# Optimization experiments

Measured on AMD Instinct MI355X. Metric: run time of the kernel, lower is better.

The kernel has to match this reference:

```python
import jax, jax.numpy as jnp
import numpy as np

BN_EPS = 1e-5
BIND_CHAN = 4  # hparams.MODEL.LEARNABLE_OFFSET.BIND_CHAN


def conv1x1(x, w, b):
    # x: [B,C,H,W], w: [O,C], b: [O]
    return jnp.einsum('bchw,oc->bohw', x, w) + b[None, :, None, None]


def bn_train(x, gamma, beta):
    # training-mode batch norm over (B,H,W) per channel
    mean = jnp.mean(x, axis=(0, 2, 3), keepdims=True)
    var = jnp.var(x, axis=(0, 2, 3), keepdims=True)
    xn = (x - mean) * jax.lax.rsqrt(var + BN_EPS)
    return xn * gamma[None, :, None, None] + beta[None, :, None, None]


def displace_channel(x, offsets):
    # x: [B,C,H,W]; offsets: [C,2] (dy,dx) per channel, continuous.
    # out[b,c,y,x] = bilinear sample of x[b,c] at (y+dy_c, x+dx_c), zeros outside.
    B, C, H, W = x.shape
    dy, dx = offsets[:, 0], offsets[:, 1]
    fy, fx = jnp.floor(dy), jnp.floor(dx)
    wy, wx = dy - fy, dx - fx          # fractional weights, [C]
    iy, ix = fy.astype(jnp.int32), fx.astype(jnp.int32)
    chan = jnp.arange(C)[:, None, None]

    def shifted(oy, ox):
        ys = jnp.arange(H)[None, :] + oy[:, None]   # [C,H]
        xs = jnp.arange(W)[None, :] + ox[:, None]   # [C,W]
        valid = ((ys >= 0) & (ys < H))[:, :, None] & ((xs >= 0) & (xs < W))[:, None, :]
        ysc = jnp.clip(ys, 0, H - 1)
        xsc = jnp.clip(xs, 0, W - 1)
        g = x[:, chan, ysc[:, :, None], xsc[:, None, :]]   # [B,C,H,W]
        return g * valid.astype(x.dtype)[None]

    w00 = ((1 - wy) * (1 - wx))[None, :, None, None]
    w01 = ((1 - wy) * wx)[None, :, None, None]
    w10 = (wy * (1 - wx))[None, :, None, None]
    w11 = (wy * wx)[None, :, None, None]
    return (w00 * shifted(iy, ix) + w01 * shifted(iy, ix + 1)
            + w10 * shifted(iy + 1, ix) + w11 * shifted(iy + 1, ix + 1))


def setup_inputs() -> dict:
    key = jax.random.key(0)
    ks = jax.random.split(key, 12)
    B, Cin, H, W = 16, 64, 128, 128
    Cd, Cout = 128, 64
    n_off = Cd // BIND_CHAN  # 32
    s_in = 1.0 / np.sqrt(Cin)
    s_d = 1.0 / np.sqrt(Cd)
    return {
        'x': jax.random.normal(ks[0], (B, Cin, H, W), jnp.float32),
        'pre_w': jax.random.uniform(ks[1], (Cd, Cin), jnp.float32, -s_in, s_in),
        'pre_b': jax.random.uniform(ks[2], (Cd,), jnp.float32, -s_in, s_in),
        'post_w': jax.random.uniform(ks[3], (Cout, Cd), jnp.float32, -s_d, s_d),
        'post_b': jax.random.uniform(ks[4], (Cout,), jnp.float32, -s_d, s_d),
        'atten_w': jax.random.uniform(ks[5], (Cd, Cin), jnp.float32, -s_in, s_in),
        'atten_b': jax.random.uniform(ks[6], (Cd,), jnp.float32, -s_in, s_in),
        'atten_bn_g': jnp.ones((Cd,), jnp.float32),
        'atten_bn_b': jnp.zeros((Cd,), jnp.float32),
        'offsets': jax.random.normal(ks[7], (n_off, 2), jnp.float32) * 3.0,
        'bn_g': jnp.ones((Cout,), jnp.float32),
        'bn_b': jnp.zeros((Cout,), jnp.float32),
    }


def reference(x, pre_w, pre_b, post_w, post_b, atten_w, atten_b,
              atten_bn_g, atten_bn_b, offsets, bn_g, bn_b):
    # pre_offset conv1x1
    out_pre = conv1x1(x, pre_w, pre_b)                        # [B,Cd,H,W]
    # DisplaceChannel: each offset shared by BIND_CHAN consecutive channels
    off_per_chan = jnp.repeat(offsets, BIND_CHAN, axis=0)     # [Cd,2]
    out_dis = displace_channel(out_pre, off_per_chan)
    # Attention branch: conv1x1 -> BN -> Softplus -> SpaceNormalization
    a = conv1x1(x, atten_w, atten_b)
    a = bn_train(a, atten_bn_g, atten_bn_b)
    a = jax.nn.softplus(a)
    out_atten = a / jnp.sum(a, axis=(2, 3), keepdims=True)    # spatial normalization
    # post_offset conv1x1 on gated displaced features
    out_post = conv1x1(out_atten * out_dis, post_w, post_b)
    # residual (inplanes == outplanes, stride 1 -> no downsample) + BN + ReLU
    out_skip = x + out_post
    return jax.nn.relu(bn_train(out_skip, bn_g, bn_b))
```

## Files before the change

kernel.cpp:

```cpp
#include <hip/hip_runtime.h>

#define HWSZ   16384
#define CIN    64
#define CD     128
#define COUT   64
#define BN_EPS 1e-5f

typedef __attribute__((ext_vector_type(8))) short short8x;
typedef __attribute__((ext_vector_type(4))) float floatx4;

#define WS_ASTAT 25344
#define WS_OSTAT 27392
#define WS_BIG   32768
#define WS_TOTAL_BYTES ((size_t)(32768 + 16777216) * 4)

__device__ __forceinline__ unsigned short f2bf(float f) {
    unsigned int u = __float_as_uint(f);
    u += 0x7fff + ((u >> 16) & 1);
    return (unsigned short)(u >> 16);
}
__device__ __forceinline__ float bf2f(unsigned short s) {
    return __uint_as_float(((unsigned int)s) << 16);
}
__device__ __forceinline__ float softplus_fast(float x) {
    return fmaxf(x, 0.f) + __logf(1.f + __expf(-fabsf(x)));
}
__device__ __forceinline__ float block_reduce(float v, float* sc) {
    #pragma unroll
    for (int off = 32; off >= 1; off >>= 1) v += __shfl_xor(v, off, 64);
    int wv = threadIdx.x >> 6, ln = threadIdx.x & 63;
    int nw = blockDim.x >> 6;
    if (ln == 0) sc[wv] = v;
    __syncthreads();
    float r = ((int)threadIdx.x < nw) ? sc[threadIdx.x] : 0.f;
    r += __shfl_xor(r, 1, 64);
    r += __shfl_xor(r, 2, 64);
    r += __shfl_xor(r, 4, 64);
    return r;
}

__device__ __forceinline__ short8x cvt_w8(const float* src) {
    float4 f0 = *(const float4*)(src);
    float4 f1 = *(const float4*)(src + 4);
    short8x w;
    w[0] = (short)f2bf(f0.x); w[1] = (short)f2bf(f0.y);
    w[2] = (short)f2bf(f0.z); w[3] = (short)f2bf(f0.w);
    w[4] = (short)f2bf(f1.x); w[5] = (short)f2bf(f1.y);
    w[6] = (short)f2bf(f1.z); w[7] = (short)f2bf(f1.w);
    return w;
}

#define OBPAD 68

__device__ __forceinline__ void pre_write_lds(unsigned short* wbuf, int c, int wv,
                                              const float4 ld[4]) {
    #pragma unroll
    for (int k = 0; k < 4; ++k) {
        int px = wv * 16 + k * 4;
        wbuf[(px + 0) * 72 + c] = f2bf(ld[k].x);
        wbuf[(px + 1) * 72 + c] = f2bf(ld[k].y);
        wbuf[(px + 2) * 72 + c] = f2bf(ld[k].z);
        wbuf[(px + 3) * 72 + c] = f2bf(ld[k].w);
    }
}

__device__ __forceinline__ void pre_compute_tile(
        const unsigned short* buf, unsigned short* ob, int ln, int wv,
        const short8x wfrag[4][2], const float bv[4]) {
    floatx4 acc[4][4];
    #pragma unroll
    for (int oi = 0; oi < 4; ++oi)
        #pragma unroll
        for (int pi = 0; pi < 4; ++pi)
            acc[oi][pi] = floatx4{bv[oi], bv[oi], bv[oi], bv[oi]};
    #pragma unroll
    for (int kk = 0; kk < 2; ++kk)
        #pragma unroll
        for (int pi = 0; pi < 4; ++pi) {
            short8x xfrag = *(const short8x*)((const char*)buf +
                    (pi * 16 + (ln & 15)) * 144 + (kk * 32 + (ln >> 4) * 8) * 2);
            #pragma unroll
            for (int oi = 0; oi < 4; ++oi)
                acc[oi][pi] = __builtin_amdgcn_mfma_f32_16x16x32_bf16(
                        xfrag, wfrag[oi][kk], acc[oi][pi], 0, 0, 0);
        }
    #pragma unroll
    for (int oi = 0; oi < 4; ++oi) {
        int row = wv * 64 + oi * 16 + (ln & 15);
        #pragma unroll
        for (int pi = 0; pi < 4; ++pi) {
            int px = pi * 16 + (ln >> 4) * 4;
            ushort4 v;
            v.x = f2bf(acc[oi][pi][0]); v.y = f2bf(acc[oi][pi][1]);
            v.z = f2bf(acc[oi][pi][2]); v.w = f2bf(acc[oi][pi][3]);
            *(ushort4*)&ob[row * OBPAD + px] = v;
        }
    }
}

__global__ __launch_bounds__(256) void conv_pre_mfma(
        const float* __restrict__ x, const float* __restrict__ pre_w,
        const float* __restrict__ atten_w,
        const float* __restrict__ pre_b, const float* __restrict__ atten_b,
        unsigned short* __restrict__ out_pre, unsigned short* __restrict__ a_out,
        float* __restrict__ a_stats8) {
    __shared__ unsigned short xT[2][64 * 72];
    __shared__ unsigned short ob[256 * OBPAD];
    int t = threadIdx.x;
    int wv = t >> 6, ln = t & 63;
    int b = blockIdx.x >> 6;
    int poff = (blockIdx.x & 63) << 8;
    const float* xg = x + (size_t)b * CIN * HWSZ + poff;
    int c = ln;

    int o0 = wv * 64;
    short8x wfrag[4][2];
    #pragma unroll
    for (int oi = 0; oi < 4; ++oi)
        #pragma unroll
        for (int kk = 0; kk < 2; ++kk) {
            int row = o0 + oi * 16 + (ln & 15);
            int kcol = kk * 32 + (ln >> 4) * 8;
            const float* wsrc = (row < 128) ? (pre_w + row * 64)
                                            : (atten_w + (row - 128) * 64);
            wfrag[oi][kk] = cvt_w8(wsrc + kcol);
        }
    float bv[4];
    #pragma unroll
    for (int oi = 0; oi < 4; ++oi) {
        int og = o0 + oi * 16;
        bv[oi] = (og < 128) ? pre_b[og + (ln & 15)] : atten_b[og - 128 + (ln & 15)];
    }

    float asum[4] = {0.f, 0.f, 0.f, 0.f};
    float asq[4]  = {0.f, 0.f, 0.f, 0.f};

    float4 lda[4], ldb[4];
    #pragma unroll
    for (int k = 0; k < 4; ++k)
        lda[k] = *(const float4*)(xg + (size_t)c * HWSZ + 0 * 64 + wv * 16 + k * 4);
    pre_write_lds(xT[0], c, wv, lda);
    #pragma unroll
    for (int k = 0; k < 4; ++k)
        lda[k] = *(const float4*)(xg + (size_t)c * HWSZ + 1 * 64 + wv * 16 + k * 4);
    __syncthreads();

    #pragma unroll
    for (int tt = 0; tt < 4; ++tt) {
        if (tt == 0) {
            #pragma unroll
            for (int k = 0; k < 4; ++k)
                ldb[k] = *(const float4*)(xg + (size_t)c * HWSZ + 2 * 64 + wv * 16 + k * 4);
        } else if (tt == 1) {
            #pragma unroll
            for (int k = 0; k < 4; ++k)
                lda[k] = *(const float4*)(xg + (size_t)c * HWSZ + 3 * 64 + wv * 16 + k * 4);
        }
        pre_compute_tile(xT[tt & 1], ob, ln, wv, wfrag, bv);
        if (tt == 0)      pre_write_lds(xT[1], c, wv, lda);
        else if (tt == 1) pre_write_lds(xT[0], c, wv, ldb);
        else if (tt == 2) pre_write_lds(xT[1], c, wv, lda);
        __syncthreads();
        int ptile = poff + tt * 64;
        #pragma unroll
        for (int j = 0; j < 8; ++j) {
            int row = j * 32 + (t >> 3);
            int px  = (t & 7) * 8;
            uint4 v = *(const uint4*)&ob[row * OBPAD + px];
            unsigned short* dst = (row < 128) ? out_pre : a_out;
            int o = row & 127;
            *(uint4*)(dst + ((size_t)b * CD + o) * HWSZ + ptile + px) = v;
            if (j >= 4) {
                unsigned int u[4] = {v.x, v.y, v.z, v.w};
                float s = 0.f, q = 0.f;
                #pragma unroll
                for (int k = 0; k < 4; ++k) {
                    float lo = bf2f((unsigned short)(u[k] & 0xffff));
                    float hi = bf2f((unsigned short)(u[k] >> 16));
                    s += lo + hi;
                    q += lo * lo + hi * hi;
                }
                asum[j - 4] += s;
                asq[j - 4]  += q;
            }
        }
        __syncthreads();
    }
    float* slot = a_stats8 + (blockIdx.x & 7) * 256;
    #pragma unroll
    for (int jj = 0; jj < 4; ++jj) {
        float s = asum[jj], q = asq[jj];
        s += __shfl_xor(s, 1, 64); q += __shfl_xor(q, 1, 64);
        s += __shfl_xor(s, 2, 64); q += __shfl_xor(q, 2, 64);
        s += __shfl_xor(s, 4, 64); q += __shfl_xor(q, 4, 64);
        if ((t & 7) == 0) {
            int o = (jj + 4) * 32 + (t >> 3) - 128;
            atomicAdd(&slot[2 * o],     s);
            atomicAdd(&slot[2 * o + 1], q);
        }
    }
}

__global__ __launch_bounds__(256) void chan_stats_bf16(
        const unsigned short* __restrict__ src, float* __restrict__ stats) {
    __shared__ float sc1[8], sc2[8];
    int c = blockIdx.x, b = blockIdx.y;
    const unsigned short* base = src + ((size_t)b * CD + c) * HWSZ;
    int t = threadIdx.x;
    float sum = 0.f, sq = 0.f;
    #pragma unroll
    for (int i = 0; i < 8; ++i) {
        uint4 v = *(const uint4*)(base + i * 2048 + t * 8);
        unsigned int u[4] = {v.x, v.y, v.z, v.w};
        #pragma unroll
        for (int k = 0; k < 4; ++k) {
            float lo = bf2f((unsigned short)(u[k] & 0xffff));
            float hi = bf2f((unsigned short)(u[k] >> 16));
            sum += lo + hi;
            sq  += lo * lo + hi * hi;
        }
    }
    sum = block_reduce(sum, sc1);
    __syncthreads();
    sq = block_reduce(sq, sc2);
    if (t == 0) {
        atomicAdd(&stats[c * 2 + 0], sum);
        atomicAdd(&stats[c * 2 + 1], sq);
    }
}

struct Win9 { float v0,v1,v2,v3,v4,v5,v6,v7,v8; };
__device__ __forceinline__ Win9 extract9(uint4 qa, uint4 qb, bool s4, int sh) {
    unsigned long long A0 = ((unsigned long long)qa.y << 32) | qa.x;
    unsigned long long A1 = ((unsigned long long)qa.w << 32) | qa.z;
    unsigned long long A2 = ((unsigned long long)qb.y << 32) | qb.x;
    unsigned long long A3 = ((unsigned long long)qb.w << 32) | qb.z;
    unsigned long long B0 = s4 ? A1 : A0;
    unsigned long long B1 = s4 ? A2 : A1;
    unsigned long long B2 = s4 ? A3 : A2;
    unsigned long long r0 = sh ? ((B0 >> sh) | (B1 << (64 - sh))) : B0;
    unsigned long long r1 = sh ? ((B1 >> sh) | (B2 << (64 - sh))) : B1;
    unsigned int v8w = (unsigned int)(sh ? (B2 >> sh) : B2);
    Win9 w;
    w.v0 = bf2f((unsigned short)(r0 >>  0)); w.v1 = bf2f((unsigned short)(r0 >> 16));
    w.v2 = bf2f((unsigned short)(r0 >> 32)); w.v3 = bf2f((unsigned short)(r0 >> 48));
    w.v4 = bf2f((unsigned short)(r1 >>  0)); w.v5 = bf2f((unsigned short)(r1 >> 16));
    w.v6 = bf2f((unsigned short)(r1 >> 32)); w.v7 = bf2f((unsigned short)(r1 >> 48));
    w.v8 = bf2f((unsigned short)(v8w & 0xffff));
    return w;
}

__global__ __launch_bounds__(512) void displace_bnsp_mul(
        unsigned short* __restrict__ pre, const unsigned short* __restrict__ a_raw,
        const float* __restrict__ stats8, const float* __restrict__ g,
        const float* __restrict__ bb, const float* __restrict__ offsets) {
    __shared__ unsigned short img[128 * 136];
    __shared__ float sc[8];
    __shared__ float s_inv;
    int bc = blockIdx.x;
    int cc = bc & 127;
    float dy = offsets[(cc >> 2) * 2 + 0];
    float dx = offsets[(cc >> 2) * 2 + 1];
    float fy = floorf(dy), fx = floorf(dx);
    float wy = dy - fy, wx = dx - fx;
    int iy = (int)fy, ix = (int)fx;
    float w00 = (1.f - wy) * (1.f - wx);
    float w01 = (1.f - wy) * wx;
    float w10 = wy * (1.f - wx);
    float w11 = wy * wx;
    float sum = 0.f, sq = 0.f;
    #pragma unroll
    for (int k = 0; k < 8; ++k) {
        sum += stats8[k * 256 + 2 * cc];
        sq  += stats8[k * 256 + 2 * cc + 1];
    }
    const float N = 262144.f;
    float mean = sum / N;
    float var  = sq / N - mean * mean;
    float rstd = rsqrtf(var + BN_EPS);
    float scl = rstd * g[cc];
    float shf = bb[cc] - mean * scl;
    unsigned short* pb = pre + (size_t)bc * HWSZ;
    const unsigned short* ab = a_raw + (size_t)bc * HWSZ;
    int t = threadIdx.x;
    float aspf[4][8];
    float lsum = 0.f;
    #pragma unroll
    for (int i = 0; i < 4; ++i) {
        int px = i * 4096 + t * 8;
        uint4 v = *(const uint4*)(pb + px);
        int y = px >> 7, xx = px & 127;
        *(uint4*)&img[y * 136 + xx] = v;
        uint4 av = *(const uint4*)(ab + px);
        unsigned int au[4] = {av.x, av.y, av.z, av.w};
        #pragma unroll
        for (int k = 0; k < 4; ++k) {
            float lo = softplus_fast(bf2f((unsigned short)(au[k] & 0xffff)) * scl + shf);
            float hi = softplus_fast(bf2f((unsigned short)(au[k] >> 16))    * scl + shf);
            lsum += lo + hi;
            aspf[i][2 * k]     = lo;
            aspf[i][2 * k + 1] = hi;
        }
    }
    lsum = block_reduce(lsum, sc);
    if (t == 0) s_inv = 1.f / lsum;
    __syncthreads();
    float inv = s_inv;
    w00 *= inv; w01 *= inv; w10 *= inv; w11 *= inv;
    int s = ix & 7;
    int ix8 = ix - s;
    int sh = (s & 3) * 16;
    bool s4 = s >= 4;
    #pragma unroll
    for (int i = 0; i < 4; ++i) {
        int px = i * 4096 + t * 8;
        int y = px >> 7, x0 = px & 127;
        int yy0 = y + iy, yy1 = yy0 + 1;
        float wA0 = (yy0 >= 0 && yy0 < 128) ? w00 : 0.f;
        float wA1 = (yy0 >= 0 && yy0 < 128) ? w01 : 0.f;
        float wB0 = (yy1 >= 0 && yy1 < 128) ? w10 : 0.f;
        float wB1 = (yy1 >= 0 && yy1 < 128) ? w11 : 0.f;
        int yc0 = min(max(yy0, 0), 127), yc1 = min(max(yy1, 0), 127);
        int w0 = x0 + ix8;
        uint4 z = {0u, 0u, 0u, 0u};
        uint4 qa0 = (w0 >= 0 && w0 <= 120)         ? *(const uint4*)&img[yc0 * 136 + w0]     : z;
        uint4 qa1 = (w0 + 8 >= 0 && w0 + 8 <= 120) ? *(const uint4*)&img[yc0 * 136 + w0 + 8] : z;
        uint4 qb0 = (w0 >= 0 && w0 <= 120)         ? *(const uint4*)&img[yc1 * 136 + w0]     : z;
        uint4 qb1 = (w0 + 8 >= 0 && w0 + 8 <= 120) ? *(const uint4*)&img[yc1 * 136 + w0 + 8] : z;
        Win9 va = extract9(qa0, qa1, s4, sh);
        Win9 vb = extract9(qb0, qb1, s4, sh);
        float m0 = (wA0*va.v0 + wA1*va.v1 + wB0*vb.v0 + wB1*vb.v1) * aspf[i][0];
        float m1 = (wA0*va.v1 + wA1*va.v2 + wB0*vb.v1 + wB1*vb.v2) * aspf[i][1];
        float m2 = (wA0*va.v2 + wA1*va.v3 + wB0*vb.v2 + wB1*vb.v3) * aspf[i][2];
        float m3 = (wA0*va.v3 + wA1*va.v4 + wB0*vb.v3 + wB1*vb.v4) * aspf[i][3];
        float m4 = (wA0*va.v4 + wA1*va.v5 + wB0*vb.v4 + wB1*vb.v5) * aspf[i][4];
        float m5 = (wA0*va.v5 + wA1*va.v6 + wB0*vb.v5 + wB1*vb.v6) * aspf[i][5];
        float m6 = (wA0*va.v6 + wA1*va.v7 + wB0*vb.v6 + wB1*vb.v7) * aspf[i][6];
        float m7 = (wA0*va.v7 + wA1*va.v8 + wB0*vb.v7 + wB1*vb.v8) * aspf[i][7];
        uint4 o;
        o.x = (unsigned int)f2bf(m0) | ((unsigned int)f2bf(m1) << 16);
        o.y = (unsigned int)f2bf(m2) | ((unsigned int)f2bf(m3) << 16);
        o.z = (unsigned int)f2bf(m4) | ((unsigned int)f2bf(m5) << 16);
        o.w = (unsigned int)f2bf(m6) | ((unsigned int)f2bf(m7) << 16);
        *(uint4*)(pb + px) = o;
    }
}

__global__ __launch_bounds__(256) void conv_post_mfma(
        const unsigned short* __restrict__ m, const float* __restrict__ post_w,
        const float* __restrict__ post_b, const float* __restrict__ x,
        unsigned short* __restrict__ skipS) {
    __shared__ unsigned short mT[128 * 128];
    int t = threadIdx.x;
    int P0 = blockIdx.x * 128;
    int b = P0 >> 14, poff = P0 & 16383;
    int cl = t & 31, q = t >> 5;
    #pragma unroll
    for (int pass = 0; pass < 4; ++pass) {
        int c = cl + pass * 32;
        const unsigned short* mrow = m + ((size_t)b * CD + c) * HWSZ + poff;
        #pragma unroll
        for (int h = 0; h < 2; ++h) {
            int px0 = h * 64 + q * 8;
            uint4 v = *(const uint4*)(mrow + px0);
            unsigned int u[4] = {v.x, v.y, v.z, v.w};
            #pragma unroll
            for (int j = 0; j < 8; ++j) {
                unsigned short val = (unsigned short)((u[j >> 1] >> ((j & 1) * 16)) & 0xffff);
                int byteoff = (px0 + j) * 256 + ((c * 2) ^ (j << 4));
                *(unsigned short*)((char*)mT + byteoff) = val;
            }
        }
    }
    __syncthreads();
    int ln = t & 63, wv = t >> 6;
    int o0 = (wv >> 1) * 32;
    int ph = (wv & 1) * 64;
    short8x aw[2][4];
    #pragma unroll
    for (int oi = 0; oi < 2; ++oi)
        #pragma unroll
        for (int kk = 0; kk < 4; ++kk) {
            int o = o0 + oi * 16 + (ln & 15);
            aw[oi][kk] = cvt_w8(post_w + o * 128 + kk * 32 + (ln >> 4) * 8);
        }
    floatx4 acc[2][4];
    #pragma unroll
    for (int oi = 0; oi < 2; ++oi)
        #pragma unroll
        for (int pi = 0; pi < 4; ++pi) acc[oi][pi] = floatx4{0.f, 0.f, 0.f, 0.f};
    #pragma unroll
    for (int kk = 0; kk < 4; ++kk)
        #pragma unroll
        for (int pi = 0; pi < 4; ++pi) {
            int px = ph + pi * 16 + (ln & 15);
            int cb = kk * 64 + (ln >> 4) * 16;
            short8x bf = *(const short8x*)((const char*)mT + px * 256 + (cb ^ ((px & 7) << 4)));
            #pragma unroll
            for (int oi = 0; oi < 2; ++oi)
                acc[oi][pi] = __builtin_amdgcn_mfma_f32_16x16x32_bf16(aw[oi][kk], bf, acc[oi][pi], 0, 0, 0);
        }
    #pragma unroll
    for (int oi = 0; oi < 2; ++oi) {
        float4 b4 = *(const float4*)(post_b + o0 + oi * 16 + (ln >> 4) * 4);
        float bb[4] = {b4.x, b4.y, b4.z, b4.w};
        #pragma unroll
        for (int pi = 0; pi < 4; ++pi) {
            int pxg = poff + ph + pi * 16 + (ln & 15);
            #pragma unroll
            for (int r = 0; r < 4; ++r) {
                int o = o0 + oi * 16 + (ln >> 4) * 4 + r;
                float val = acc[oi][pi][r] + bb[r] + x[((size_t)b * COUT + o) * HWSZ + pxg];
                skipS[((size_t)b * CD + o) * HWSZ + pxg] = f2bf(val);
            }
        }
    }
}

__global__ __launch_bounds__(256) void bn_relu_out(
        const unsigned short* __restrict__ skipS, float* __restrict__ out,
        const float* __restrict__ stats, const float* __restrict__ g,
        const float* __restrict__ bb) {
    const float N = 262144.f;
    int t = threadIdx.x;
    #pragma unroll
    for (int k = 0; k < 4; ++k) {
        size_t gidx = (size_t)blockIdx.x * 1024 + k * 256 + t;
        size_t e = gidx * 8;
        int b = (int)(e >> 20);
        int c = (int)(e >> 14) & 63;
        int px = (int)(e & 16383);
        float mean = stats[c * 2] / N;
        float rstd = rsqrtf(stats[c * 2 + 1] / N - mean * mean + BN_EPS);
        float gc = g[c], bbc = bb[c];
        uint4 v = *(const uint4*)(skipS + ((size_t)b * CD + c) * HWSZ + px);
        unsigned int u[4] = {v.x, v.y, v.z, v.w};
        float4 o0, o1;
        float* op[8] = {&o0.x, &o0.y, &o0.z, &o0.w, &o1.x, &o1.y, &o1.z, &o1.w};
        #pragma unroll
        for (int j = 0; j < 8; ++j) {
            float val = bf2f((unsigned short)((u[j >> 1] >> ((j & 1) * 16)) & 0xffff));
            *op[j] = fmaxf((val - mean) * rstd * gc + bbc, 0.f);
        }
        *(float4*)(out + e) = o0;
        *(float4*)(out + e + 4) = o1;
    }
}

extern "C" void kernel_launch(void* const* d_in, const int* in_sizes, int n_in,
                              void* d_out, int out_size, void* d_ws, size_t ws_size,
                              hipStream_t stream) {
    const float* x          = (const float*)d_in[0];
    const float* pre_w      = (const float*)d_in[1];
    const float* pre_b      = (const float*)d_in[2];
    const float* post_w     = (const float*)d_in[3];
    const float* post_b     = (const float*)d_in[4];
    const float* atten_w    = (const float*)d_in[5];
    const float* atten_b    = (const float*)d_in[6];
    const float* atten_bn_g = (const float*)d_in[7];
    const float* atten_bn_b = (const float*)d_in[8];
    const float* offsets    = (const float*)d_in[9];
    const float* bn_g       = (const float*)d_in[10];
    const float* bn_b       = (const float*)d_in[11];
    float* out = (float*)d_out;
    float* ws  = (float*)d_ws;

    if (ws_size < WS_TOTAL_BYTES) return;

    float* a_stats8 = ws + WS_ASTAT;
    float* o_stats  = ws + WS_OSTAT;
    unsigned short* big   = (unsigned short*)(ws + WS_BIG);
    unsigned short* a_buf = (unsigned short*)d_out;

    hipMemsetAsync((void*)a_stats8, 0, (2048 + 128) * sizeof(float), stream);

    conv_pre_mfma<<<1024, 256, 0, stream>>>(x, pre_w, atten_w, pre_b, atten_b, big, a_buf, a_stats8);
    displace_bnsp_mul<<<2048, 512, 0, stream>>>(big, a_buf, a_stats8, atten_bn_g, atten_bn_b, offsets);
    conv_post_mfma<<<2048, 256, 0, stream>>>(big, post_w, post_b, x, big);
    chan_stats_bf16<<<dim3(64, 16), 256, 0, stream>>>(big, o_stats);
    bn_relu_out<<<2048, 256, 0, stream>>>(big, out, o_stats, bn_g, bn_b);
}
```

Measured before the change: 152.7 us.

## Fuse output BN statistics into post conv and coalesce its epilogue via LDS

Removes the separate chan_stats_bf16 pass by computing per-channel sum and sum-of-squares in the conv_post epilogue, accumulating into 8 striped atomic slots that bn_relu_out then sums. The MFMA operand order is swapped so each lane holds consecutive pixels for one output channel. Results are staged through a padded LDS tile so x is read as float4 and skipS is written as 16-byte rows. This saves a full re-read of the 32 MB bf16 intermediate and one kernel launch, at the cost of extra LDS, a barrier and more atomics per block.

```diff
diff --git a/kernel.cpp b/kernel.cpp
--- a/kernel.cpp
+++ b/kernel.cpp
@@ -198,34 +198,6 @@
             atomicAdd(&slot[2 * o],     s);
             atomicAdd(&slot[2 * o + 1], q);
         }
-    }
-}
-
-__global__ __launch_bounds__(256) void chan_stats_bf16(
-        const unsigned short* __restrict__ src, float* __restrict__ stats) {
-    __shared__ float sc1[8], sc2[8];
-    int c = blockIdx.x, b = blockIdx.y;
-    const unsigned short* base = src + ((size_t)b * CD + c) * HWSZ;
-    int t = threadIdx.x;
-    float sum = 0.f, sq = 0.f;
-    #pragma unroll
-    for (int i = 0; i < 8; ++i) {
-        uint4 v = *(const uint4*)(base + i * 2048 + t * 8);
-        unsigned int u[4] = {v.x, v.y, v.z, v.w};
-        #pragma unroll
-        for (int k = 0; k < 4; ++k) {
-            float lo = bf2f((unsigned short)(u[k] & 0xffff));
-            float hi = bf2f((unsigned short)(u[k] >> 16));
-            sum += lo + hi;
-            sq  += lo * lo + hi * hi;
-        }
-    }
-    sum = block_reduce(sum, sc1);
-    __syncthreads();
-    sq = block_reduce(sq, sc2);
-    if (t == 0) {
-        atomicAdd(&stats[c * 2 + 0], sum);
-        atomicAdd(&stats[c * 2 + 1], sq);
     }
 }
 
@@ -346,11 +318,13 @@
     }
 }
 
+#define OPPAD 132
 __global__ __launch_bounds__(256) void conv_post_mfma(
         const unsigned short* __restrict__ m, const float* __restrict__ post_w,
         const float* __restrict__ post_b, const float* __restrict__ x,
-        unsigned short* __restrict__ skipS) {
+        unsigned short* __restrict__ skipS, float* __restrict__ o_stats8) {
     __shared__ unsigned short mT[128 * 128];
+    __shared__ unsigned short ot[64 * OPPAD];
     int t = threadIdx.x;
     int P0 = blockIdx.x * 128;
     int b = P0 >> 14, poff = P0 & 16383;
@@ -395,31 +369,67 @@
         for (int pi = 0; pi < 4; ++pi) {
             int px = ph + pi * 16 + (ln & 15);
             int cb = kk * 64 + (ln >> 4) * 16;
-            short8x bf = *(const short8x*)((const char*)mT + px * 256 + (cb ^ ((px & 7) << 4)));
+            short8x mf = *(const short8x*)((const char*)mT + px * 256 + (cb ^ ((px & 7) << 4)));
             #pragma unroll
             for (int oi = 0; oi < 2; ++oi)
-                acc[oi][pi] = __builtin_amdgcn_mfma_f32_16x16x32_bf16(aw[oi][kk], bf, acc[oi][pi], 0, 0, 0);
+                acc[oi][pi] = __builtin_amdgcn_mfma_f32_16x16x32_bf16(mf, aw[oi][kk], acc[oi][pi], 0, 0, 0);
         }
     #pragma unroll
     for (int oi = 0; oi < 2; ++oi) {
-        float4 b4 = *(const float4*)(post_b + o0 + oi * 16 + (ln >> 4) * 4);
-        float bb[4] = {b4.x, b4.y, b4.z, b4.w};
+        int o = o0 + oi * 16 + (ln & 15);
+        float bvp = post_b[o];
         #pragma unroll
         for (int pi = 0; pi < 4; ++pi) {
-            int pxg = poff + ph + pi * 16 + (ln & 15);
-            #pragma unroll
-            for (int r = 0; r < 4; ++r) {
-                int o = o0 + oi * 16 + (ln >> 4) * 4 + r;
-                float val = acc[oi][pi][r] + bb[r] + x[((size_t)b * COUT + o) * HWSZ + pxg];
-                skipS[((size_t)b * CD + o) * HWSZ + pxg] = f2bf(val);
-            }
+            int pxl = ph + pi * 16 + (ln >> 4) * 4;
+            float4 xv = *(const float4*)(x + ((size_t)b * COUT + o) * HWSZ + poff + pxl);
+            ushort4 sv;
+            sv.x = f2bf(acc[oi][pi][0] + bvp + xv.x);
+            sv.y = f2bf(acc[oi][pi][1] + bvp + xv.y);
+            sv.z = f2bf(acc[oi][pi][2] + bvp + xv.z);
+            sv.w = f2bf(acc[oi][pi][3] + bvp + xv.w);
+            *(ushort4*)&ot[o * OPPAD + pxl] = sv;
+        }
+    }
+    __syncthreads();
+    float osum[4] = {0.f, 0.f, 0.f, 0.f};
+    float osq[4]  = {0.f, 0.f, 0.f, 0.f};
+    #pragma unroll
+    for (int j = 0; j < 4; ++j) {
+        int o  = j * 16 + (t >> 4);
+        int px = (t & 15) * 8;
+        uint4 v = *(const uint4*)&ot[o * OPPAD + px];
+        *(uint4*)(skipS + ((size_t)b * CD + o) * HWSZ + poff + px) = v;
+        unsigned int u[4] = {v.x, v.y, v.z, v.w};
+        float s = 0.f, q = 0.f;
+        #pragma unroll
+        for (int k = 0; k < 4; ++k) {
+            float lo = bf2f((unsigned short)(u[k] & 0xffff));
+            float hi = bf2f((unsigned short)(u[k] >> 16));
+            s += lo + hi;
+            q += lo * lo + hi * hi;
+        }
+        osum[j] += s;
+        osq[j]  += q;
+    }
+    float* slot = o_stats8 + (blockIdx.x & 7) * 128;
+    #pragma unroll
+    for (int j = 0; j < 4; ++j) {
+        float s = osum[j], q = osq[j];
+        s += __shfl_xor(s, 1, 64); q += __shfl_xor(q, 1, 64);
+        s += __shfl_xor(s, 2, 64); q += __shfl_xor(q, 2, 64);
+        s += __shfl_xor(s, 4, 64); q += __shfl_xor(q, 4, 64);
+        s += __shfl_xor(s, 8, 64); q += __shfl_xor(q, 8, 64);
+        if ((t & 15) == 0) {
+            int o = j * 16 + (t >> 4);
+            atomicAdd(&slot[2 * o],     s);
+            atomicAdd(&slot[2 * o + 1], q);
         }
     }
 }
 
 __global__ __launch_bounds__(256) void bn_relu_out(
         const unsigned short* __restrict__ skipS, float* __restrict__ out,
-        const float* __restrict__ stats, const float* __restrict__ g,
+        const float* __restrict__ stats8, const float* __restrict__ g,
         const float* __restrict__ bb) {
     const float N = 262144.f;
     int t = threadIdx.x;
@@ -430,8 +440,14 @@
         int b = (int)(e >> 20);
         int c = (int)(e >> 14) & 63;
         int px = (int)(e & 16383);
-        float mean = stats[c * 2] / N;
-        float rstd = rsqrtf(stats[c * 2 + 1] / N - mean * mean + BN_EPS);
+        float sum = 0.f, sq = 0.f;
+        #pragma unroll
+        for (int kk = 0; kk < 8; ++kk) {
+            sum += stats8[kk * 128 + 2 * c];
+            sq  += stats8[kk * 128 + 2 * c + 1];
+        }
+        float mean = sum / N;
+        float rstd = rsqrtf(sq / N - mean * mean + BN_EPS);
         float gc = g[c], bbc = bb[c];
         uint4 v = *(const uint4*)(skipS + ((size_t)b * CD + c) * HWSZ + px);
         unsigned int u[4] = {v.x, v.y, v.z, v.w};
@@ -468,15 +484,14 @@
     if (ws_size < WS_TOTAL_BYTES) return;
 
     float* a_stats8 = ws + WS_ASTAT;
-    float* o_stats  = ws + WS_OSTAT;
+    float* o_stats8 = ws + WS_OSTAT;
     unsigned short* big   = (unsigned short*)(ws + WS_BIG);
     unsigned short* a_buf = (unsigned short*)d_out;
 
-    hipMemsetAsync((void*)a_stats8, 0, (2048 + 128) * sizeof(float), stream);
+    hipMemsetAsync((void*)a_stats8, 0, (2048 + 1024) * sizeof(float), stream);
 
     conv_pre_mfma<<<1024, 256, 0, stream>>>(x, pre_w, atten_w, pre_b, atten_b, big, a_buf, a_stats8);
     displace_bnsp_mul<<<2048, 512, 0, stream>>>(big, a_buf, a_stats8, atten_bn_g, atten_bn_b, offsets);
-    conv_post_mfma<<<2048, 256, 0, stream>>>(big, post_w, post_b, x, big);
-    chan_stats_bf16<<<dim3(64, 16), 256, 0, stream>>>(big, o_stats);
-    bn_relu_out<<<2048, 256, 0, stream>>>(big, out, o_stats, bn_g, bn_b);
-}
+    conv_post_mfma<<<2048, 256, 0, stream>>>(big, post_w, post_b, x, big, o_stats8);
+    bn_relu_out<<<2048, 256, 0, stream>>>(big, out, o_stats8, bn_g, bn_b);
+}
```

Measured after the change: 151.4 us, median of 2. About the same (-0.9%).
